# Kernel tuning notes

Hardware: AMD Instinct MI355X
Metric: run time of the kernel (lower is better)

## Reference

```python
import jax, jax.numpy as jnp
import numpy as np

EPS = 1e-16  # matches PyG softmax denominator epsilon


def setup_inputs() -> dict:
    key = jax.random.key(0)
    k1, k2, k3, k4 = jax.random.split(key, 4)
    N, F, G = 200000, 256, 1024
    x = jax.random.normal(k1, (N, F), dtype=jnp.float32)
    batch = jnp.sort(jax.random.randint(k2, (N,), 0, G, dtype=jnp.int64))
    Wg = jax.random.normal(k3, (F, 1), dtype=jnp.float32) / np.sqrt(F)
    bg = jnp.zeros((1,), dtype=jnp.float32)
    Wn = jax.random.normal(k4, (F, F), dtype=jnp.float32) / np.sqrt(F)
    bn = jnp.zeros((F,), dtype=jnp.float32)
    return {"x": x, "batch": batch, "size": G, "Wg": Wg, "bg": bg, "Wn": Wn, "bn": bn}


def reference(x, batch, size, Wg, bg, Wn, bn):
    # gate scores: [N, 1]
    gate = x @ Wg + bg
    # transformed features: [N, F]
    h = x @ Wn + bn
    # per-graph (segment) softmax over gate, numerically stable
    seg_max = jax.ops.segment_max(gate, batch, num_segments=size)  # [G, 1]
    e = jnp.exp(gate - seg_max[batch])                             # [N, 1]
    seg_sum = jax.ops.segment_sum(e, batch, num_segments=size)     # [G, 1]
    alpha = e / (seg_sum[batch] + EPS)                             # [N, 1]
    # weighted scatter-add: [G, F]
    out = jax.ops.segment_sum(alpha * h, batch, num_segments=size)
    return out
```

## Files before the change

### kernel.cpp

```cpp
#include <hip/hip_runtime.h>
#include <math.h>

#define FDIM 256
#define EPSF 1e-16f

typedef float f32x4 __attribute__((ext_vector_type(4)));

__device__ __forceinline__ float dot4v(f32x4 a, f32x4 b) {
    return a.x * b.x + a.y * b.y + a.z * b.z + a.w * b.w;
}

__device__ __forceinline__ f32x4 ntload(const float* p) {
    return __builtin_nontemporal_load(reinterpret_cast<const f32x4*>(p));
}

__global__ void __launch_bounds__(256) k_ranges(const int* __restrict__ batch,
                                                int* __restrict__ seg_start,
                                                int N, int G) {
    int i = blockIdx.x * blockDim.x + threadIdx.x;
    if (i > N) return;
    int b  = (i == N) ? G : batch[i];
    int bp = (i == 0) ? -1 : batch[i - 1];
    for (int g = bp + 1; g <= b; ++g) seg_start[g] = i;
}

__global__ void __launch_bounds__(512) k_fused(const int* __restrict__ seg_start,
                                               const float* __restrict__ x,
                                               const float* __restrict__ Wg,
                                               float* __restrict__ yn,
                                               float* __restrict__ alpha) {
    int g = blockIdx.x;
    int rs = seg_start[g];
    int re = seg_start[g + 1];

    __shared__ float s_s[32];
    __shared__ float s_acc[32][FDIM];

    int part = threadIdx.x >> 4;
    int l16  = threadIdx.x & 15;

    const f32x4 wg0 = *reinterpret_cast<const f32x4*>(Wg +   0 + l16 * 4);
    const f32x4 wg1 = *reinterpret_cast<const f32x4*>(Wg +  64 + l16 * 4);
    const f32x4 wg2 = *reinterpret_cast<const f32x4*>(Wg + 128 + l16 * 4);
    const f32x4 wg3 = *reinterpret_cast<const f32x4*>(Wg + 192 + l16 * 4);

    f32x4 a0 = (f32x4)0.f, a1 = (f32x4)0.f, a2 = (f32x4)0.f, a3 = (f32x4)0.f;
    float s = 0.f;

    int r = rs + part;
    for (; r + 32 < re; r += 64) {
        const float* rp0 = x + (size_t)r * FDIM;
        const float* rp1 = x + (size_t)(r + 32) * FDIM;
        f32x4 x0 = ntload(rp0 +   0 + l16 * 4);
        f32x4 x1 = ntload(rp0 +  64 + l16 * 4);
        f32x4 x2 = ntload(rp0 + 128 + l16 * 4);
        f32x4 x3 = ntload(rp0 + 192 + l16 * 4);
        f32x4 y0 = ntload(rp1 +   0 + l16 * 4);
        f32x4 y1 = ntload(rp1 +  64 + l16 * 4);
        f32x4 y2 = ntload(rp1 + 128 + l16 * 4);
        f32x4 y3 = ntload(rp1 + 192 + l16 * 4);
        float d0 = dot4v(x0, wg0) + dot4v(x1, wg1) + dot4v(x2, wg2) + dot4v(x3, wg3);
        float d1 = dot4v(y0, wg0) + dot4v(y1, wg1) + dot4v(y2, wg2) + dot4v(y3, wg3);
        #pragma unroll
        for (int off = 1; off < 16; off <<= 1) {
            d0 += __shfl_xor(d0, off, 64);
            d1 += __shfl_xor(d1, off, 64);
        }
        float w0 = __expf(d0);
        float w1 = __expf(d1);
        a0 += w0 * x0; a1 += w0 * x1; a2 += w0 * x2; a3 += w0 * x3;
        a0 += w1 * y0; a1 += w1 * y1; a2 += w1 * y2; a3 += w1 * y3;
        s += w0 + w1;
    }
    if (r < re) {
        const float* rp = x + (size_t)r * FDIM;
        f32x4 x0 = ntload(rp +   0 + l16 * 4);
        f32x4 x1 = ntload(rp +  64 + l16 * 4);
        f32x4 x2 = ntload(rp + 128 + l16 * 4);
        f32x4 x3 = ntload(rp + 192 + l16 * 4);
        float d = dot4v(x0, wg0) + dot4v(x1, wg1) + dot4v(x2, wg2) + dot4v(x3, wg3);
        #pragma unroll
        for (int off = 1; off < 16; off <<= 1) d += __shfl_xor(d, off, 64);
        float w = __expf(d);
        a0 += w * x0; a1 += w * x1; a2 += w * x2; a3 += w * x3;
        s += w;
    }

    *reinterpret_cast<f32x4*>(&s_acc[part][  0 + l16 * 4]) = a0;
    *reinterpret_cast<f32x4*>(&s_acc[part][ 64 + l16 * 4]) = a1;
    *reinterpret_cast<f32x4*>(&s_acc[part][128 + l16 * 4]) = a2;
    *reinterpret_cast<f32x4*>(&s_acc[part][192 + l16 * 4]) = a3;
    if (l16 == 0) s_s[part] = s;
    __syncthreads();

    if (threadIdx.x < FDIM) {
        int c = threadIdx.x;
        float v = 0.f;
        #pragma unroll
        for (int p = 0; p < 32; ++p) v += s_acc[p][c];
        float tot = 0.f;
        #pragma unroll
        for (int p = 0; p < 32; ++p) tot += s_s[p];
        float inv = 1.0f / (tot + EPSF);
        yn[(size_t)g * FDIM + c] = v * inv;
        if (c == 0) alpha[g] = tot * inv;
    }
}

__global__ void __launch_bounds__(512) k4s(const float* __restrict__ yn,
                                           const float* __restrict__ alpha,
                                           const float* __restrict__ Wn,
                                           const float* __restrict__ bn,
                                           float* __restrict__ out, int G) {
    int bx = blockIdx.x & 3;
    int by = blockIdx.x >> 2;
    int r = threadIdx.x >> 6;
    int c = bx * 64 + (threadIdx.x & 63);
    int g = by * 8 + r;
    if (g >= G) return;
    const float* yrow = yn + (size_t)g * FDIM;
    const float* wcol = Wn + c;
    float acc = 0.f;
    #pragma unroll 8
    for (int k = 0; k < FDIM; ++k)
        acc = fmaf(yrow[k], wcol[(size_t)k * FDIM], acc);
    out[(size_t)g * FDIM + c] = acc + alpha[g] * bn[c];
}

extern "C" void kernel_launch(void* const* d_in, const int* in_sizes, int n_in,
                              void* d_out, int out_size, void* d_ws, size_t ws_size,
                              hipStream_t stream) {
    const float* x     = (const float*)d_in[0];
    const int*   batch = (const int*)d_in[1];
    const float* Wg    = (const float*)d_in[3];
    const float* Wn    = (const float*)d_in[5];
    const float* bn    = (const float*)d_in[6];
    float* out = (float*)d_out;

    int N = in_sizes[1];
    int G = out_size / FDIM;

    int*   seg_start = (int*)d_ws;
    float* alpha = (float*)(seg_start + ((G + 2) & ~1));
    float* yn = alpha + G;

    k_ranges<<<(N + 1 + 255) / 256, 256, 0, stream>>>(batch, seg_start, N, G);
    k_fused<<<G, 512, 0, stream>>>(seg_start, x, Wg, yn, alpha);
    k4s<<<((G + 7) / 8) * 4, 512, 0, stream>>>(yn, alpha, Wn, bn, out, G);
}
```

Baseline: 58.63 us.

## Split segment reduction into fixed row tiles with per-tile partial sums

The fused gate/softmax/accumulate kernel now gives each block a fixed tile of 98 rows instead of one whole graph segment. Each block writes per-segment partial weighted sums and exp-sums into up to 8 slots. The output kernel combines the partials for each graph, normalises them, and does the Wn projection from shared memory. This is meant to fix load imbalance from uneven segment sizes and raise the block count. The costs are an extra partial-buffer round trip, a loss of the 2-row unrolling, and a slot clamp that gives wrong results if a tile spans more than 8 segments.

```diff
diff --git a/kernel.cpp b/kernel.cpp
--- a/kernel.cpp
+++ b/kernel.cpp
@@ -3,6 +3,8 @@
 
 #define FDIM 256
 #define EPSF 1e-16f
+#define TILE 98
+#define SLOTS 8
 
 typedef float f32x4 __attribute__((ext_vector_type(4)));
 
@@ -24,17 +26,18 @@
     for (int g = bp + 1; g <= b; ++g) seg_start[g] = i;
 }
 
-__global__ void __launch_bounds__(512) k_fused(const int* __restrict__ seg_start,
+__global__ void __launch_bounds__(256) k_fused(const int* __restrict__ seg_start,
+                                               const int* __restrict__ batch,
                                                const float* __restrict__ x,
                                                const float* __restrict__ Wg,
-                                               float* __restrict__ yn,
-                                               float* __restrict__ alpha) {
-    int g = blockIdx.x;
-    int rs = seg_start[g];
-    int re = seg_start[g + 1];
+                                               float* __restrict__ part_y,
+                                               float* __restrict__ part_s, int N) {
+    int b = blockIdx.x;
+    int rs_t = b * TILE;
+    int re_t = min(N, rs_t + TILE);
 
-    __shared__ float s_s[32];
-    __shared__ float s_acc[32][FDIM];
+    __shared__ float s_s[16];
+    __shared__ float s_acc[16][FDIM];
 
     int part = threadIdx.x >> 4;
     int l16  = threadIdx.x & 15;
@@ -44,87 +47,99 @@
     const f32x4 wg2 = *reinterpret_cast<const f32x4*>(Wg + 128 + l16 * 4);
     const f32x4 wg3 = *reinterpret_cast<const f32x4*>(Wg + 192 + l16 * 4);
 
-    f32x4 a0 = (f32x4)0.f, a1 = (f32x4)0.f, a2 = (f32x4)0.f, a3 = (f32x4)0.f;
-    float s = 0.f;
+    int g = batch[rs_t];
+    int lo = rs_t;
+    int slot = 0;
 
-    int r = rs + part;
-    for (; r + 32 < re; r += 64) {
-        const float* rp0 = x + (size_t)r * FDIM;
-        const float* rp1 = x + (size_t)(r + 32) * FDIM;
-        f32x4 x0 = ntload(rp0 +   0 + l16 * 4);
-        f32x4 x1 = ntload(rp0 +  64 + l16 * 4);
-        f32x4 x2 = ntload(rp0 + 128 + l16 * 4);
-        f32x4 x3 = ntload(rp0 + 192 + l16 * 4);
-        f32x4 y0 = ntload(rp1 +   0 + l16 * 4);
-        f32x4 y1 = ntload(rp1 +  64 + l16 * 4);
-        f32x4 y2 = ntload(rp1 + 128 + l16 * 4);
-        f32x4 y3 = ntload(rp1 + 192 + l16 * 4);
-        float d0 = dot4v(x0, wg0) + dot4v(x1, wg1) + dot4v(x2, wg2) + dot4v(x3, wg3);
-        float d1 = dot4v(y0, wg0) + dot4v(y1, wg1) + dot4v(y2, wg2) + dot4v(y3, wg3);
+    while (lo < re_t) {
+        int hi = min(re_t, seg_start[g + 1]);
+
+        f32x4 a0 = (f32x4)0.f, a1 = (f32x4)0.f, a2 = (f32x4)0.f, a3 = (f32x4)0.f;
+        float s = 0.f;
+        for (int r = lo + part; r < hi; r += 16) {
+            const float* rp = x + (size_t)r * FDIM;
+            f32x4 x0 = ntload(rp +   0 + l16 * 4);
+            f32x4 x1 = ntload(rp +  64 + l16 * 4);
+            f32x4 x2 = ntload(rp + 128 + l16 * 4);
+            f32x4 x3 = ntload(rp + 192 + l16 * 4);
+            float d = dot4v(x0, wg0) + dot4v(x1, wg1) + dot4v(x2, wg2) + dot4v(x3, wg3);
+            #pragma unroll
+            for (int off = 1; off < 16; off <<= 1) d += __shfl_xor(d, off, 64);
+            float w = __expf(d);
+            a0 += w * x0; a1 += w * x1; a2 += w * x2; a3 += w * x3;
+            s += w;
+        }
+
+        *reinterpret_cast<f32x4*>(&s_acc[part][  0 + l16 * 4]) = a0;
+        *reinterpret_cast<f32x4*>(&s_acc[part][ 64 + l16 * 4]) = a1;
+        *reinterpret_cast<f32x4*>(&s_acc[part][128 + l16 * 4]) = a2;
+        *reinterpret_cast<f32x4*>(&s_acc[part][192 + l16 * 4]) = a3;
+        if (l16 == 0) s_s[part] = s;
+        __syncthreads();
+
+        int c = threadIdx.x;
+        float Y = 0.f;
         #pragma unroll
-        for (int off = 1; off < 16; off <<= 1) {
-            d0 += __shfl_xor(d0, off, 64);
-            d1 += __shfl_xor(d1, off, 64);
+        for (int p = 0; p < 16; ++p) Y += s_acc[p][c];
+        part_y[((size_t)b * SLOTS + slot) * FDIM + c] = Y;
+        if (c == 0) {
+            float S = 0.f;
+            #pragma unroll
+            for (int p = 0; p < 16; ++p) S += s_s[p];
+            part_s[b * SLOTS + slot] = S;
         }
-        float w0 = __expf(d0);
-        float w1 = __expf(d1);
-        a0 += w0 * x0; a1 += w0 * x1; a2 += w0 * x2; a3 += w0 * x3;
-        a0 += w1 * y0; a1 += w1 * y1; a2 += w1 * y2; a3 += w1 * y3;
-        s += w0 + w1;
-    }
-    if (r < re) {
-        const float* rp = x + (size_t)r * FDIM;
-        f32x4 x0 = ntload(rp +   0 + l16 * 4);
-        f32x4 x1 = ntload(rp +  64 + l16 * 4);
-        f32x4 x2 = ntload(rp + 128 + l16 * 4);
-        f32x4 x3 = ntload(rp + 192 + l16 * 4);
-        float d = dot4v(x0, wg0) + dot4v(x1, wg1) + dot4v(x2, wg2) + dot4v(x3, wg3);
-        #pragma unroll
-        for (int off = 1; off < 16; off <<= 1) d += __shfl_xor(d, off, 64);
-        float w = __expf(d);
-        a0 += w * x0; a1 += w * x1; a2 += w * x2; a3 += w * x3;
-        s += w;
-    }
+        __syncthreads();
 
-    *reinterpret_cast<f32x4*>(&s_acc[part][  0 + l16 * 4]) = a0;
-    *reinterpret_cast<f32x4*>(&s_acc[part][ 64 + l16 * 4]) = a1;
-    *reinterpret_cast<f32x4*>(&s_acc[part][128 + l16 * 4]) = a2;
-    *reinterpret_cast<f32x4*>(&s_acc[part][192 + l16 * 4]) = a3;
-    if (l16 == 0) s_s[part] = s;
-    __syncthreads();
-
-    if (threadIdx.x < FDIM) {
-        int c = threadIdx.x;
-        float v = 0.f;
-        #pragma unroll
-        for (int p = 0; p < 32; ++p) v += s_acc[p][c];
-        float tot = 0.f;
-        #pragma unroll
-        for (int p = 0; p < 32; ++p) tot += s_s[p];
-        float inv = 1.0f / (tot + EPSF);
-        yn[(size_t)g * FDIM + c] = v * inv;
-        if (c == 0) alpha[g] = tot * inv;
+        lo = hi;
+        ++g;
+        slot = min(slot + 1, SLOTS - 1);
     }
 }
 
-__global__ void __launch_bounds__(512) k4s(const float* __restrict__ yn,
-                                           const float* __restrict__ alpha,
-                                           const float* __restrict__ Wn,
-                                           const float* __restrict__ bn,
-                                           float* __restrict__ out, int G) {
-    int bx = blockIdx.x & 3;
-    int by = blockIdx.x >> 2;
-    int r = threadIdx.x >> 6;
-    int c = bx * 64 + (threadIdx.x & 63);
-    int g = by * 8 + r;
-    if (g >= G) return;
-    const float* yrow = yn + (size_t)g * FDIM;
-    const float* wcol = Wn + c;
-    float acc = 0.f;
-    #pragma unroll 8
-    for (int k = 0; k < FDIM; ++k)
-        acc = fmaf(yrow[k], wcol[(size_t)k * FDIM], acc);
-    out[(size_t)g * FDIM + c] = acc + alpha[g] * bn[c];
+__global__ void __launch_bounds__(1024) k4_out(const int* __restrict__ seg_start,
+                                               const int* __restrict__ batch,
+                                               const float* __restrict__ part_y,
+                                               const float* __restrict__ part_s,
+                                               const float* __restrict__ Wn,
+                                               const float* __restrict__ bn,
+                                               float* __restrict__ out, int G, int N) {
+    int r = threadIdx.x >> 8;
+    int c = threadIdx.x & 255;
+    int g = blockIdx.x * 4 + r;
+
+    __shared__ float ys[4][FDIM];
+    __shared__ float s_alpha[4];
+
+    if (g < G) {
+        int rs = seg_start[g], re = seg_start[g + 1];
+        float Y = 0.f, S = 0.f;
+        if (re > rs) {
+            int tb0 = rs / TILE, tb1 = (re - 1) / TILE;
+            for (int tb = tb0; tb <= tb1; ++tb) {
+                int slot = min(g - batch[tb * TILE], SLOTS - 1);
+                Y += part_y[((size_t)tb * SLOTS + slot) * FDIM + c];
+                S += part_s[tb * SLOTS + slot];
+            }
+        }
+        float inv = 1.0f / (S + EPSF);
+        ys[r][c] = Y * inv;
+        if (c == 0) s_alpha[r] = S * inv;
+    } else {
+        ys[r][c] = 0.f;
+        if (c == 0) s_alpha[r] = 0.f;
+    }
+    __syncthreads();
+
+    float acc0 = 0.f, acc1 = 0.f, acc2 = 0.f, acc3 = 0.f;
+    #pragma unroll 4
+    for (int k = 0; k < FDIM; k += 4) {
+        acc0 = fmaf(ys[r][k    ], Wn[(k    ) * FDIM + c], acc0);
+        acc1 = fmaf(ys[r][k + 1], Wn[(k + 1) * FDIM + c], acc1);
+        acc2 = fmaf(ys[r][k + 2], Wn[(k + 2) * FDIM + c], acc2);
+        acc3 = fmaf(ys[r][k + 3], Wn[(k + 3) * FDIM + c], acc3);
+    }
+    if (g < G)
+        out[(size_t)g * FDIM + c] = (acc0 + acc1) + (acc2 + acc3) + s_alpha[r] * bn[c];
 }
 
 extern "C" void kernel_launch(void* const* d_in, const int* in_sizes, int n_in,
@@ -139,12 +154,14 @@
 
     int N = in_sizes[1];
     int G = out_size / FDIM;
+    int ntiles = (N + TILE - 1) / TILE;
 
     int*   seg_start = (int*)d_ws;
-    float* alpha = (float*)(seg_start + ((G + 2) & ~1));
-    float* yn = alpha + G;
+    float* part_s = (float*)(seg_start + ((G + 2) & ~1));
+    float* part_y = part_s + (size_t)ntiles * SLOTS;
 
     k_ranges<<<(N + 1 + 255) / 256, 256, 0, stream>>>(batch, seg_start, N, G);
-    k_fused<<<G, 512, 0, stream>>>(seg_start, x, Wg, yn, alpha);
-    k4s<<<((G + 7) / 8) * 4, 512, 0, stream>>>(yn, alpha, Wn, bn, out, G);
+    k_fused<<<ntiles, 256, 0, stream>>>(seg_start, batch, x, Wg, part_y, part_s, N);
+    k4_out<<<(G + 3) / 4, 1024, 0, stream>>>(seg_start, batch, part_y, part_s,
+                                             Wn, bn, out, G, N);
 }
```

After: 56.93 us. 2.9% less time.
